# Kernel tuning notes

Hardware: AMD Instinct MI355X
Metric: run time of the kernel (lower is better)

## Reference

```python
import jax, jax.numpy as jnp
import numpy as np

N = 10000
E = 320000

def gcn_layer(x, W, edge_src, edge_dst, edge_weight):
    # support = x @ W ; out = spmm(adj, support) via edge-list scatter-add
    support = x @ W                                  # [N, H]
    msgs = edge_weight[:, None] * support[edge_src]  # [E, H] gather (irregular)
    return jax.ops.segment_sum(msgs, edge_dst, num_segments=N)

def setup_inputs() -> dict:
    key = jax.random.key(0)
    ks = jax.random.split(key, 7)
    F_in, H1, H2 = 3000, 512, 64
    x = jax.random.normal(ks[0], (N, F_in), dtype=jnp.float32)
    edge_src = jax.random.randint(ks[1], (E,), 0, N)
    edge_dst = jax.random.randint(ks[2], (E,), 0, N)
    edge_weight = jax.random.uniform(ks[3], (E,), dtype=jnp.float32)
    W1 = jax.random.normal(ks[4], (F_in, H1), dtype=jnp.float32) * (1.0 / np.sqrt(F_in))
    W2 = jax.random.normal(ks[5], (H1, H2), dtype=jnp.float32) * (1.0 / np.sqrt(H1))
    W3 = jax.random.normal(ks[6], (H1, H2), dtype=jnp.float32) * (1.0 / np.sqrt(H1))
    return {"x": x, "edge_src": edge_src, "edge_dst": edge_dst,
            "edge_weight": edge_weight, "W1": W1, "W2": W2, "W3": W3}

def reference(x, edge_src, edge_dst, edge_weight, W1, W2, W3):
    # Eval mode: dropout is identity, reparameterize returns mu.
    h1 = jax.nn.relu(gcn_layer(x, W1, edge_src, edge_dst, edge_weight))  # [N, H1]
    mu = gcn_layer(h1, W2, edge_src, edge_dst, edge_weight)              # [N, H2]
    logvar = gcn_layer(h1, W3, edge_src, edge_dst, edge_weight)          # [N, H2]
    z = mu
    pred = z @ z.T  # InnerProductDecoder with act = identity -> [N, N]
    return (pred, mu, logvar)
```

## Files before the change

kernel.cpp:

```cpp
#include <hip/hip_runtime.h>
#include <hip/hip_bf16.h>

#define N_NODES 10000
#define N_EDGES 320000
#define F_IN    3000
#define KP      3008
#define H1      512
#define H2      64
#define CAP     128
#define NT      (KP / 32)

typedef float  f32x4  __attribute__((ext_vector_type(4)));
typedef short  bf16x8 __attribute__((ext_vector_type(8)));
typedef unsigned short us8 __attribute__((ext_vector_type(8)));

__device__ __forceinline__ unsigned short f2b(float f) {
    union { float f; unsigned u; } v; v.f = f;
    unsigned r = v.u + 0x7FFF + ((v.u >> 16) & 1);
    return (unsigned short)(r >> 16);
}
__device__ __forceinline__ float b2f(unsigned short b) {
    union { unsigned u; float f; } v; v.u = ((unsigned)b) << 16;
    return v.f;
}

#define GLOAD_LDS16(gptr, lptr)                                                             \
    __builtin_amdgcn_global_load_lds((const __attribute__((address_space(1))) void*)(gptr), \
                                     (__attribute__((address_space(3))) void*)(lptr),       \
                                     16, 0, 0)

#define NB_BUCKET 1250
#define NB_CONVX  14688
#define NB_CONVW  376

__global__ __launch_bounds__(256) void prep(const int* __restrict__ src,
                                            const int* __restrict__ dst,
                                            const float* __restrict__ w,
                                            const float* __restrict__ x,
                                            const float* __restrict__ W1,
                                            int* __restrict__ cnt,
                                            int* __restrict__ bsrc,
                                            float* __restrict__ bw,
                                            unsigned short* __restrict__ xb,
                                            unsigned short* __restrict__ w1t) {
    __shared__ float tr[64][65];
    const int b = blockIdx.x;
    const int t = threadIdx.x;
    if (b < NB_BUCKET) {
        int e = b * 256 + t;
        if (e >= N_EDGES) return;
        int d = dst[e];
        int slot = atomicAdd(&cnt[d], 1);
        if (slot < CAP) {
            bsrc[d * CAP + slot] = src[e];
            bw[d * CAP + slot]   = w[e];
        }
    } else if (b < NB_BUCKET + NB_CONVX) {
        int idx = (b - NB_BUCKET) * 256 + t;
        int r = idx / (KP / 8);
        int g = idx % (KP / 8);
        if (r >= N_NODES) return;
        us8 v;
        if (g * 8 + 8 <= F_IN) {
            float4 a = *(const float4*)&x[(size_t)r * F_IN + g * 8];
            float4 c = *(const float4*)&x[(size_t)r * F_IN + g * 8 + 4];
            v[0] = f2b(a.x); v[1] = f2b(a.y); v[2] = f2b(a.z); v[3] = f2b(a.w);
            v[4] = f2b(c.x); v[5] = f2b(c.y); v[6] = f2b(c.z); v[7] = f2b(c.w);
        } else {
            #pragma unroll
            for (int j = 0; j < 8; ++j) {
                int k = g * 8 + j;
                v[j] = (k < F_IN) ? f2b(x[(size_t)r * F_IN + k]) : (unsigned short)0;
            }
        }
        *(us8*)&xb[(size_t)r * KP + g * 8] = v;
    } else {
        int bb = b - NB_BUCKET - NB_CONVX;
        int kBase = (bb >> 3) * 64;
        int cBase = (bb & 7) * 64;
        int col = cBase + (t & 63);
        #pragma unroll
        for (int i = 0; i < 16; ++i) {
            int row = kBase + i * 4 + (t >> 6);
            float v = (row < F_IN) ? W1[(size_t)row * H1 + col] : 0.f;
            tr[t & 63][i * 4 + (t >> 6)] = v;
        }
        __syncthreads();
        int c = t >> 2, kq = (t & 3) * 16;
        us8 o0, o1;
        #pragma unroll
        for (int j = 0; j < 8; ++j) { o0[j] = f2b(tr[c][kq + j]); o1[j] = f2b(tr[c][kq + 8 + j]); }
        *(us8*)&w1t[(size_t)(cBase + c) * KP + kBase + kq]     = o0;
        *(us8*)&w1t[(size_t)(cBase + c) * KP + kBase + kq + 8] = o1;
    }
}

__global__ __launch_bounds__(256) void gemm1_mfma(const unsigned short* __restrict__ xb,
                                                  const unsigned short* __restrict__ w1t,
                                                  unsigned short* __restrict__ Cb) {
    __shared__ unsigned short As[2][128 * 32];
    __shared__ unsigned short Bs[2][64 * 32];
    const int f  = blockIdx.x;
    const int k8 = f & 7;
    const int j  = f >> 3;
    const int bx = k8 * 10 + (j >> 3);
    const int by = j & 7;
    const int mBase = bx * 128;
    const int nBase = by * 64;

    const int t = threadIdx.x;
    const int wid = t >> 6, lane = t & 63;
    const int wr = (wid >> 1) * 64;
    const int wc = (wid & 1) * 32;
    const int fr = lane & 15;
    const int fk = (lane >> 4) * 8;

    const int arow0 = min(mBase + wid * 16 + (lane >> 2), N_NODES - 1);
    const int arow1 = min(mBase + (wid + 4) * 16 + (lane >> 2), N_NODES - 1);
    const int brow  = nBase + wid * 16 + (lane >> 2);
    const int kq    = (lane & 3) * 8;

    f32x4 acc[4][2] = {};

#define STAGE1(c, k0)                                                          \
    do {                                                                       \
        GLOAD_LDS16(&xb[(size_t)arow0 * KP + (k0) + kq], &As[c][wid * 512]);   \
        GLOAD_LDS16(&xb[(size_t)arow1 * KP + (k0) + kq], &As[c][(wid + 4) * 512]); \
        GLOAD_LDS16(&w1t[(size_t)brow * KP + (k0) + kq], &Bs[c][wid * 512]);   \
    } while (0)

#define COMPUTE1(c)                                                            \
    do {                                                                       \
        bf16x8 af[4], bfv[2];                                                  \
        _Pragma("unroll")                                                      \
        for (int m = 0; m < 4; ++m)                                            \
            af[m] = *(const bf16x8*)&As[c][(wr + m * 16 + fr) * 32 + fk];      \
        _Pragma("unroll")                                                      \
        for (int n = 0; n < 2; ++n)                                            \
            bfv[n] = *(const bf16x8*)&Bs[c][(wc + n * 16 + fr) * 32 + fk];     \
        _Pragma("unroll")                                                      \
        for (int m = 0; m < 4; ++m)                                            \
            _Pragma("unroll")                                                  \
            for (int n = 0; n < 2; ++n)                                        \
                acc[m][n] = __builtin_amdgcn_mfma_f32_16x16x32_bf16(af[m], bfv[n], acc[m][n], 0, 0, 0); \
    } while (0)

    STAGE1(0, 0);
    __syncthreads();
    int cur = 0;
    for (int tt = 0; tt < NT - 1; ++tt) {
        STAGE1(cur ^ 1, (tt + 1) * 32);
        COMPUTE1(cur);
        __syncthreads();
        cur ^= 1;
    }
    COMPUTE1(cur);

#undef STAGE1
#undef COMPUTE1

    #pragma unroll
    for (int m = 0; m < 4; ++m) {
        int rbase = mBase + wr + m * 16 + (lane >> 4) * 4;
        #pragma unroll
        for (int n = 0; n < 2; ++n) {
            int col = nBase + wc + n * 16 + (lane & 15);
            #pragma unroll
            for (int i = 0; i < 4; ++i) {
                int row = rbase + i;
                if (row < N_NODES)
                    Cb[(size_t)row * H1 + col] = f2b(acc[m][n][i]);
            }
        }
    }
}

__global__ __launch_bounds__(256) void gather_h1(const unsigned short* __restrict__ sup,
                                                 const int* __restrict__ cnt,
                                                 const int* __restrict__ bsrc,
                                                 const float* __restrict__ bw,
                                                 float* __restrict__ h1) {
    const int wid  = threadIdx.x >> 6;
    const int lane = threadIdx.x & 63;
    const int n    = blockIdx.x * 4 + wid;
    const int deg  = min(cnt[n], CAP);
    float acc[8] = {};
    for (int e = 0; e < deg; ++e) {
        int   s = bsrc[n * CAP + e];
        float w = bw[n * CAP + e];
        us8 v = *(const us8*)&sup[(size_t)s * H1 + lane * 8];
        #pragma unroll
        for (int j = 0; j < 8; ++j) acc[j] += w * b2f(v[j]);
    }
    float4 o0 = make_float4(fmaxf(acc[0], 0.f), fmaxf(acc[1], 0.f), fmaxf(acc[2], 0.f), fmaxf(acc[3], 0.f));
    float4 o1 = make_float4(fmaxf(acc[4], 0.f), fmaxf(acc[5], 0.f), fmaxf(acc[6], 0.f), fmaxf(acc[7], 0.f));
    *(float4*)&h1[(size_t)n * H1 + lane * 8]     = o0;
    *(float4*)&h1[(size_t)n * H1 + lane * 8 + 4] = o1;
}

__global__ __launch_bounds__(256) void gemm_h1w23(const float* __restrict__ h1,
                                                  const float* __restrict__ W2,
                                                  const float* __restrict__ W3,
                                                  float* __restrict__ sup2) {
    __shared__ float hs[16][H1];
    const int rBase = blockIdx.x * 16;
    const int t = threadIdx.x;
    for (int idx = t * 4; idx < 16 * H1; idx += 256 * 4) {
        int r = idx >> 9;
        int k = idx & 511;
        *(float4*)&hs[r][k] = *(const float4*)&h1[(size_t)(rBase + r) * H1 + k];
    }
    __syncthreads();
    const int col = t & 127;
    const int rg  = (t >> 7) * 8;
    const float* W = (col < 64) ? (W2 + col) : (W3 + (col - 64));
    float acc[8] = {};
    for (int k = 0; k < H1; ++k) {
        float wv = W[k * 64];
        #pragma unroll
        for (int i = 0; i < 8; ++i) acc[i] += wv * hs[rg + i][k];
    }
    #pragma unroll
    for (int i = 0; i < 8; ++i)
        sup2[(size_t)(rBase + rg + i) * 128 + col] = acc[i];
}

__global__ __launch_bounds__(256) void gather_muvar(const float* __restrict__ sup2,
                                                    const int* __restrict__ cnt,
                                                    const int* __restrict__ bsrc,
                                                    const float* __restrict__ bw,
                                                    float* __restrict__ mu,
                                                    float* __restrict__ lv,
                                                    unsigned short* __restrict__ mub) {
    const int n  = blockIdx.x * 8 + (threadIdx.x >> 5);
    const int c4 = (threadIdx.x & 31) * 4;
    const int deg = min(cnt[n], CAP);
    float4 acc = make_float4(0.f, 0.f, 0.f, 0.f);
    for (int e = 0; e < deg; ++e) {
        int   s = bsrc[n * CAP + e];
        float w = bw[n * CAP + e];
        float4 v = *(const float4*)&sup2[(size_t)s * 128 + c4];
        acc.x += w * v.x; acc.y += w * v.y; acc.z += w * v.z; acc.w += w * v.w;
    }
    if (c4 < 64) {
        *(float4*)&mu[(size_t)n * 64 + c4] = acc;
        mub[(size_t)n * 64 + c4 + 0] = f2b(acc.x);
        mub[(size_t)n * 64 + c4 + 1] = f2b(acc.y);
        mub[(size_t)n * 64 + c4 + 2] = f2b(acc.z);
        mub[(size_t)n * 64 + c4 + 3] = f2b(acc.w);
    } else {
        *(float4*)&lv[(size_t)n * 64 + (c4 - 64)] = acc;
    }
}

__global__ __launch_bounds__(256) void pred_mfma(const unsigned short* __restrict__ mub,
                                                 float* __restrict__ pred) {
    __shared__ float st[4][16][68];
    const int t = threadIdx.x, wid = t >> 6, lane = t & 63;
    const int rb = blockIdx.x * 128 + (wid >> 1) * 64;
    const int cb = blockIdx.y * 128 + (wid & 1) * 64;
    const int fr = lane & 15, fk = (lane >> 4) * 8;
    f32x4 acc[4][4] = {};

    #pragma unroll
    for (int ks = 0; ks < 2; ++ks) {
        bf16x8 af[4], bfv[4];
        #pragma unroll
        for (int m = 0; m < 4; ++m) {
            int r = min(rb + m * 16 + fr, N_NODES - 1);
            af[m] = *(const bf16x8*)&mub[(size_t)r * 64 + ks * 32 + fk];
        }
        #pragma unroll
        for (int n = 0; n < 4; ++n) {
            int c = min(cb + n * 16 + fr, N_NODES - 1);
            bfv[n] = *(const bf16x8*)&mub[(size_t)c * 64 + ks * 32 + fk];
        }
        #pragma unroll
        for (int m = 0; m < 4; ++m)
            #pragma unroll
            for (int n = 0; n < 4; ++n)
                acc[m][n] = __builtin_amdgcn_mfma_f32_16x16x32_bf16(af[m], bfv[n], acc[m][n], 0, 0, 0);
    }

    #pragma unroll
    for (int m = 0; m < 4; ++m) {
        #pragma unroll
        for (int n = 0; n < 4; ++n)
            #pragma unroll
            for (int i = 0; i < 4; ++i)
                st[wid][(lane >> 4) * 4 + i][n * 16 + (lane & 15)] = acc[m][n][i];
        int rbase = rb + m * 16;
        #pragma unroll
        for (int it = 0; it < 4; ++it) {
            int row   = it * 4 + (lane >> 4);
            int chunk = lane & 15;
            int grow  = rbase + row;
            int gcol  = cb + chunk * 4;
            if (grow < N_NODES) {
                f32x4 v = *(const f32x4*)&st[wid][row][chunk * 4];
                if (gcol + 3 < N_NODES) {
                    __builtin_nontemporal_store(v, (f32x4*)&pred[(size_t)grow * N_NODES + gcol]);
                } else {
                    #pragma unroll
                    for (int j = 0; j < 4; ++j)
                        if (gcol + j < N_NODES)
                            __builtin_nontemporal_store(v[j], &pred[(size_t)grow * N_NODES + gcol + j]);
                }
            }
        }
    }
}

extern "C" void kernel_launch(void* const* d_in, const int* in_sizes, int n_in,
                              void* d_out, int out_size, void* d_ws, size_t ws_size,
                              hipStream_t stream) {
    const float* x    = (const float*)d_in[0];
    const int*   esrc = (const int*)d_in[1];
    const int*   edst = (const int*)d_in[2];
    const float* ew   = (const float*)d_in[3];
    const float* W1   = (const float*)d_in[4];
    const float* W2   = (const float*)d_in[5];
    const float* W3   = (const float*)d_in[6];

    float* pred = (float*)d_out;
    float* mu   = pred + (size_t)N_NODES * N_NODES;
    float* lv   = mu   + (size_t)N_NODES * H2;

    char* ws = (char*)d_ws;
    unsigned short* sup1b = (unsigned short*)ws; ws += (size_t)N_NODES * H1 * sizeof(short);
    float* h1       = (float*)ws; ws += (size_t)N_NODES * H1 * sizeof(float);
    float* support2 = (float*)ws; ws += (size_t)N_NODES * 2 * H2 * sizeof(float);
    int*   cnt      = (int*)ws;   ws += (size_t)N_NODES * sizeof(int);
    int*   bsrc     = (int*)ws;   ws += (size_t)N_NODES * CAP * sizeof(int);
    float* bw       = (float*)ws; ws += (size_t)N_NODES * CAP * sizeof(float);
    unsigned short* xb  = (unsigned short*)ws; ws += (size_t)N_NODES * KP * sizeof(short);
    unsigned short* w1t = (unsigned short*)ws; ws += (size_t)H1 * KP * sizeof(short);
    unsigned short* mub = (unsigned short*)ws; ws += (size_t)N_NODES * H2 * sizeof(short);

    (void)hipMemsetAsync(cnt, 0, N_NODES * sizeof(int), stream);
    prep<<<NB_BUCKET + NB_CONVX + NB_CONVW, 256, 0, stream>>>(esrc, edst, ew, x, W1,
                                                              cnt, bsrc, bw, xb, w1t);
    gemm1_mfma<<<640, 256, 0, stream>>>(xb, w1t, sup1b);
    gather_h1<<<N_NODES / 4, 256, 0, stream>>>(sup1b, cnt, bsrc, bw, h1);
    gemm_h1w23<<<N_NODES / 16, 256, 0, stream>>>(h1, W2, W3, support2);
    gather_muvar<<<N_NODES / 8, 256, 0, stream>>>(support2, cnt, bsrc, bw, mu, lv, mub);
    pred_mfma<<<dim3((N_NODES + 127) / 128, (N_NODES + 127) / 128), 256, 0, stream>>>(mub, pred);
}
```

Before: 344.5 us.

## Fuse x bf16 conversion into GEMM1 loads and merge gather with W2/W3 GEMM

GEMM1 now reads fp32 x directly, converts it to bf16 in registers and writes it into XOR-swizzled LDS with a K tile of 64. This removes the separate pass that materialised a padded bf16 copy of x. The layer-1 gather is also fused with the h1·[W2|W3] GEMM, so h1 stays in shared memory and never makes a round trip through global memory. In exchange, GEMM1 loads A through registers instead of direct-to-LDS loads, which raises register pressure and may expose more latency on the A operand.

```diff
diff --git a/kernel.cpp b/kernel.cpp
--- a/kernel.cpp
+++ b/kernel.cpp
@@ -8,17 +8,24 @@
 #define H1      512
 #define H2      64
 #define CAP     128
-#define NT      (KP / 32)
+#define BK1     64
+#define NT1     47
 
 typedef float  f32x4  __attribute__((ext_vector_type(4)));
 typedef short  bf16x8 __attribute__((ext_vector_type(8)));
 typedef unsigned short us8 __attribute__((ext_vector_type(8)));
+typedef unsigned int u32x2 __attribute__((ext_vector_type(2)));
 
 __device__ __forceinline__ unsigned short f2b(float f) {
     union { float f; unsigned u; } v; v.f = f;
     unsigned r = v.u + 0x7FFF + ((v.u >> 16) & 1);
     return (unsigned short)(r >> 16);
 }
+__device__ __forceinline__ unsigned short f2b_rne(float f) {
+    union { __hip_bfloat16 h; unsigned short u; } cv;
+    cv.h = __float2bfloat16(f);
+    return cv.u;
+}
 __device__ __forceinline__ float b2f(unsigned short b) {
     union { unsigned u; float f; } v; v.u = ((unsigned)b) << 16;
     return v.f;
@@ -30,18 +37,15 @@
                                      16, 0, 0)
 
 #define NB_BUCKET 1250
-#define NB_CONVX  14688
 #define NB_CONVW  376
 
 __global__ __launch_bounds__(256) void prep(const int* __restrict__ src,
                                             const int* __restrict__ dst,
                                             const float* __restrict__ w,
-                                            const float* __restrict__ x,
                                             const float* __restrict__ W1,
                                             int* __restrict__ cnt,
                                             int* __restrict__ bsrc,
                                             float* __restrict__ bw,
-                                            unsigned short* __restrict__ xb,
                                             unsigned short* __restrict__ w1t) {
     __shared__ float tr[64][65];
     const int b = blockIdx.x;
@@ -55,27 +59,8 @@
             bsrc[d * CAP + slot] = src[e];
             bw[d * CAP + slot]   = w[e];
         }
-    } else if (b < NB_BUCKET + NB_CONVX) {
-        int idx = (b - NB_BUCKET) * 256 + t;
-        int r = idx / (KP / 8);
-        int g = idx % (KP / 8);
-        if (r >= N_NODES) return;
-        us8 v;
-        if (g * 8 + 8 <= F_IN) {
-            float4 a = *(const float4*)&x[(size_t)r * F_IN + g * 8];
-            float4 c = *(const float4*)&x[(size_t)r * F_IN + g * 8 + 4];
-            v[0] = f2b(a.x); v[1] = f2b(a.y); v[2] = f2b(a.z); v[3] = f2b(a.w);
-            v[4] = f2b(c.x); v[5] = f2b(c.y); v[6] = f2b(c.z); v[7] = f2b(c.w);
-        } else {
-            #pragma unroll
-            for (int j = 0; j < 8; ++j) {
-                int k = g * 8 + j;
-                v[j] = (k < F_IN) ? f2b(x[(size_t)r * F_IN + k]) : (unsigned short)0;
-            }
-        }
-        *(us8*)&xb[(size_t)r * KP + g * 8] = v;
     } else {
-        int bb = b - NB_BUCKET - NB_CONVX;
+        int bb = b - NB_BUCKET;
         int kBase = (bb >> 3) * 64;
         int cBase = (bb & 7) * 64;
         int col = cBase + (t & 63);
@@ -95,68 +80,117 @@
     }
 }
 
-__global__ __launch_bounds__(256) void gemm1_mfma(const unsigned short* __restrict__ xb,
+__global__ __launch_bounds__(256) void gemm1_mfma(const float* __restrict__ x,
                                                   const unsigned short* __restrict__ w1t,
                                                   unsigned short* __restrict__ Cb) {
-    __shared__ unsigned short As[2][128 * 32];
-    __shared__ unsigned short Bs[2][64 * 32];
+    __shared__ unsigned short As[2][128 * BK1];
+    __shared__ unsigned short Bs[2][64 * BK1];
     const int f  = blockIdx.x;
     const int k8 = f & 7;
-    const int j  = f >> 3;
-    const int bx = k8 * 10 + (j >> 3);
-    const int by = j & 7;
+    const int jj = f >> 3;
+    const int bx = k8 * 10 + (jj >> 3);
+    const int by = jj & 7;
     const int mBase = bx * 128;
     const int nBase = by * 64;
 
     const int t = threadIdx.x;
     const int wid = t >> 6, lane = t & 63;
-    const int wr = (wid >> 1) * 64;
-    const int wc = (wid & 1) * 32;
-    const int fr = lane & 15;
-    const int fk = (lane >> 4) * 8;
-
-    const int arow0 = min(mBase + wid * 16 + (lane >> 2), N_NODES - 1);
-    const int arow1 = min(mBase + (wid + 4) * 16 + (lane >> 2), N_NODES - 1);
-    const int brow  = nBase + wid * 16 + (lane >> 2);
-    const int kq    = (lane & 3) * 8;
+    const int wr  = (wid >> 1) * 64;
+    const int wc  = (wid & 1) * 32;
+    const int fr  = lane & 15;
+    const int fkb = (lane >> 4) * 16;
+
+    const int l15 = lane & 15;
+    const int arow0 = wid * 32 + (lane >> 4);
+    const int brow_loc = wid * 16 + (lane >> 3);
+    const int bsw      = (((lane & 7) ^ (lane >> 3)) * 16);
 
     f32x4 acc[4][2] = {};
-
-#define STAGE1(c, k0)                                                          \
-    do {                                                                       \
-        GLOAD_LDS16(&xb[(size_t)arow0 * KP + (k0) + kq], &As[c][wid * 512]);   \
-        GLOAD_LDS16(&xb[(size_t)arow1 * KP + (k0) + kq], &As[c][(wid + 4) * 512]); \
-        GLOAD_LDS16(&w1t[(size_t)brow * KP + (k0) + kq], &Bs[c][wid * 512]);   \
+    float4 avf[8];
+
+#define A_LOAD(k0)                                                              \
+    do {                                                                        \
+        const int kk = (k0) + l15 * 4;                                          \
+        const bool ok = kk < F_IN;                                              \
+        _Pragma("unroll")                                                       \
+        for (int it = 0; it < 8; ++it) {                                        \
+            int r = min(mBase + arow0 + it * 4, N_NODES - 1);                   \
+            avf[it] = ok ? *(const float4*)&x[(size_t)r * F_IN + kk]            \
+                         : make_float4(0.f, 0.f, 0.f, 0.f);                     \
+        }                                                                       \
     } while (0)
 
-#define COMPUTE1(c)                                                            \
-    do {                                                                       \
-        bf16x8 af[4], bfv[2];                                                  \
-        _Pragma("unroll")                                                      \
-        for (int m = 0; m < 4; ++m)                                            \
-            af[m] = *(const bf16x8*)&As[c][(wr + m * 16 + fr) * 32 + fk];      \
-        _Pragma("unroll")                                                      \
-        for (int n = 0; n < 2; ++n)                                            \
-            bfv[n] = *(const bf16x8*)&Bs[c][(wc + n * 16 + fr) * 32 + fk];     \
-        _Pragma("unroll")                                                      \
-        for (int m = 0; m < 4; ++m)                                            \
-            _Pragma("unroll")                                                  \
-            for (int n = 0; n < 2; ++n)                                        \
-                acc[m][n] = __builtin_amdgcn_mfma_f32_16x16x32_bf16(af[m], bfv[n], acc[m][n], 0, 0, 0); \
+#define A_WRITE(buf)                                                            \
+    do {                                                                        \
+        _Pragma("unroll")                                                       \
+        for (int it = 0; it < 8; ++it) {                                        \
+            int row = arow0 + it * 4;                                           \
+            unsigned short s0 = f2b_rne(avf[it].x), s1 = f2b_rne(avf[it].y);    \
+            unsigned short s2 = f2b_rne(avf[it].z), s3 = f2b_rne(avf[it].w);    \
+            u32x2 pk; pk[0] = s0 | ((unsigned)s1 << 16);                        \
+            pk[1] = s2 | ((unsigned)s3 << 16);                                  \
+            *(u32x2*)((char*)&As[buf][0] + row * 128 +                          \
+                      ((l15 * 8) ^ ((row & 7) << 4))) = pk;                     \
+        }                                                                       \
     } while (0)
 
-    STAGE1(0, 0);
+#define B_GLOAD(buf, k0)                                                        \
+    do {                                                                        \
+        _Pragma("unroll")                                                       \
+        for (int c = 0; c < 2; ++c) {                                           \
+            const char* gb = (const char*)w1t +                                 \
+                ((size_t)(nBase + brow_loc + c * 8) * KP + (k0)) * 2 + bsw;     \
+            GLOAD_LDS16(gb, (char*)&Bs[buf][0] + wid * 2048 + c * 1024);        \
+        }                                                                       \
+    } while (0)
+
+#define COMPUTE1(buf)                                                           \
+    do {                                                                        \
+        bf16x8 af[4][2], bfv[2][2];                                             \
+        _Pragma("unroll")                                                       \
+        for (int m = 0; m < 4; ++m) {                                           \
+            int row = wr + m * 16 + fr;                                         \
+            _Pragma("unroll")                                                   \
+            for (int ks = 0; ks < 2; ++ks)                                      \
+                af[m][ks] = *(const bf16x8*)((const char*)&As[buf][0] +         \
+                    row * 128 + ((ks * 64 + fkb) ^ ((row & 7) << 4)));          \
+        }                                                                       \
+        _Pragma("unroll")                                                       \
+        for (int n = 0; n < 2; ++n) {                                           \
+            int row = wc + n * 16 + fr;                                         \
+            _Pragma("unroll")                                                   \
+            for (int ks = 0; ks < 2; ++ks)                                      \
+                bfv[n][ks] = *(const bf16x8*)((const char*)&Bs[buf][0] +        \
+                    row * 128 + ((ks * 64 + fkb) ^ ((row & 7) << 4)));          \
+        }                                                                       \
+        _Pragma("unroll")                                                       \
+        for (int ks = 0; ks < 2; ++ks)                                          \
+            _Pragma("unroll")                                                   \
+            for (int m = 0; m < 4; ++m)                                         \
+                _Pragma("unroll")                                               \
+                for (int n = 0; n < 2; ++n)                                     \
+                    acc[m][n] = __builtin_amdgcn_mfma_f32_16x16x32_bf16(        \
+                        af[m][ks], bfv[n][ks], acc[m][n], 0, 0, 0);             \
+    } while (0)
+
+    B_GLOAD(0, 0);
+    A_LOAD(0);
+    A_WRITE(0);
     __syncthreads();
     int cur = 0;
-    for (int tt = 0; tt < NT - 1; ++tt) {
-        STAGE1(cur ^ 1, (tt + 1) * 32);
+    for (int tt = 0; tt < NT1 - 1; ++tt) {
+        B_GLOAD(cur ^ 1, (tt + 1) * BK1);
+        A_LOAD((tt + 1) * BK1);
         COMPUTE1(cur);
+        A_WRITE(cur ^ 1);
         __syncthreads();
         cur ^= 1;
     }
     COMPUTE1(cur);
 
-#undef STAGE1
+#undef A_LOAD
+#undef A_WRITE
+#undef B_GLOAD
 #undef COMPUTE1
 
     #pragma unroll
@@ -175,54 +209,50 @@
     }
 }
 
-__global__ __launch_bounds__(256) void gather_h1(const unsigned short* __restrict__ sup,
-                                                 const int* __restrict__ cnt,
-                                                 const int* __restrict__ bsrc,
-                                                 const float* __restrict__ bw,
-                                                 float* __restrict__ h1) {
-    const int wid  = threadIdx.x >> 6;
-    const int lane = threadIdx.x & 63;
-    const int n    = blockIdx.x * 4 + wid;
-    const int deg  = min(cnt[n], CAP);
-    float acc[8] = {};
-    for (int e = 0; e < deg; ++e) {
-        int   s = bsrc[n * CAP + e];
-        float w = bw[n * CAP + e];
-        us8 v = *(const us8*)&sup[(size_t)s * H1 + lane * 8];
-        #pragma unroll
-        for (int j = 0; j < 8; ++j) acc[j] += w * b2f(v[j]);
-    }
-    float4 o0 = make_float4(fmaxf(acc[0], 0.f), fmaxf(acc[1], 0.f), fmaxf(acc[2], 0.f), fmaxf(acc[3], 0.f));
-    float4 o1 = make_float4(fmaxf(acc[4], 0.f), fmaxf(acc[5], 0.f), fmaxf(acc[6], 0.f), fmaxf(acc[7], 0.f));
-    *(float4*)&h1[(size_t)n * H1 + lane * 8]     = o0;
-    *(float4*)&h1[(size_t)n * H1 + lane * 8 + 4] = o1;
-}
-
-__global__ __launch_bounds__(256) void gemm_h1w23(const float* __restrict__ h1,
-                                                  const float* __restrict__ W2,
-                                                  const float* __restrict__ W3,
-                                                  float* __restrict__ sup2) {
+__global__ __launch_bounds__(512) void gather_gemm23(const unsigned short* __restrict__ sup,
+                                                     const int* __restrict__ cnt,
+                                                     const int* __restrict__ bsrc,
+                                                     const float* __restrict__ bw,
+                                                     const float* __restrict__ W2,
+                                                     const float* __restrict__ W3,
+                                                     float* __restrict__ sup2) {
     __shared__ float hs[16][H1];
+    const int t = threadIdx.x;
+    const int wid = t >> 6, lane = t & 63;
     const int rBase = blockIdx.x * 16;
-    const int t = threadIdx.x;
-    for (int idx = t * 4; idx < 16 * H1; idx += 256 * 4) {
-        int r = idx >> 9;
-        int k = idx & 511;
-        *(float4*)&hs[r][k] = *(const float4*)&h1[(size_t)(rBase + r) * H1 + k];
+
+    #pragma unroll
+    for (int i = 0; i < 2; ++i) {
+        const int local = wid * 2 + i;
+        const int n = rBase + local;
+        const int deg = min(cnt[n], CAP);
+        float acc[8] = {};
+        for (int e = 0; e < deg; ++e) {
+            int   s = bsrc[n * CAP + e];
+            float w = bw[n * CAP + e];
+            us8 v = *(const us8*)&sup[(size_t)s * H1 + lane * 8];
+            #pragma unroll
+            for (int j = 0; j < 8; ++j) acc[j] += w * b2f(v[j]);
+        }
+        *(float4*)&hs[local][lane * 8] =
+            make_float4(fmaxf(acc[0], 0.f), fmaxf(acc[1], 0.f), fmaxf(acc[2], 0.f), fmaxf(acc[3], 0.f));
+        *(float4*)&hs[local][lane * 8 + 4] =
+            make_float4(fmaxf(acc[4], 0.f), fmaxf(acc[5], 0.f), fmaxf(acc[6], 0.f), fmaxf(acc[7], 0.f));
     }
     __syncthreads();
+
     const int col = t & 127;
-    const int rg  = (t >> 7) * 8;
+    const int rg  = (t >> 7) * 4;
     const float* W = (col < 64) ? (W2 + col) : (W3 + (col - 64));
-    float acc[8] = {};
+    float acc2[4] = {};
     for (int k = 0; k < H1; ++k) {
         float wv = W[k * 64];
         #pragma unroll
-        for (int i = 0; i < 8; ++i) acc[i] += wv * hs[rg + i][k];
-    }
-    #pragma unroll
-    for (int i = 0; i < 8; ++i)
-        sup2[(size_t)(rBase + rg + i) * 128 + col] = acc[i];
+        for (int i = 0; i < 4; ++i) acc2[i] += wv * hs[rg + i][k];
+    }
+    #pragma unroll
+    for (int i = 0; i < 4; ++i)
+        sup2[(size_t)(rBase + rg + i) * 128 + col] = acc2[i];
 }
 
 __global__ __launch_bounds__(256) void gather_muvar(const float* __restrict__ sup2,
@@ -328,21 +358,17 @@
 
     char* ws = (char*)d_ws;
     unsigned short* sup1b = (unsigned short*)ws; ws += (size_t)N_NODES * H1 * sizeof(short);
-    float* h1       = (float*)ws; ws += (size_t)N_NODES * H1 * sizeof(float);
     float* support2 = (float*)ws; ws += (size_t)N_NODES * 2 * H2 * sizeof(float);
     int*   cnt      = (int*)ws;   ws += (size_t)N_NODES * sizeof(int);
     int*   bsrc     = (int*)ws;   ws += (size_t)N_NODES * CAP * sizeof(int);
     float* bw       = (float*)ws; ws += (size_t)N_NODES * CAP * sizeof(float);
-    unsigned short* xb  = (unsigned short*)ws; ws += (size_t)N_NODES * KP * sizeof(short);
     unsigned short* w1t = (unsigned short*)ws; ws += (size_t)H1 * KP * sizeof(short);
     unsigned short* mub = (unsigned short*)ws; ws += (size_t)N_NODES * H2 * sizeof(short);
 
     (void)hipMemsetAsync(cnt, 0, N_NODES * sizeof(int), stream);
-    prep<<<NB_BUCKET + NB_CONVX + NB_CONVW, 256, 0, stream>>>(esrc, edst, ew, x, W1,
-                                                              cnt, bsrc, bw, xb, w1t);
-    gemm1_mfma<<<640, 256, 0, stream>>>(xb, w1t, sup1b);
-    gather_h1<<<N_NODES / 4, 256, 0, stream>>>(sup1b, cnt, bsrc, bw, h1);
-    gemm_h1w23<<<N_NODES / 16, 256, 0, stream>>>(h1, W2, W3, support2);
+    prep<<<NB_BUCKET + NB_CONVW, 256, 0, stream>>>(esrc, edst, ew, W1, cnt, bsrc, bw, w1t);
+    gemm1_mfma<<<640, 256, 0, stream>>>(x, w1t, sup1b);
+    gather_gemm23<<<N_NODES / 16, 512, 0, stream>>>(sup1b, cnt, bsrc, bw, W2, W3, support2);
     gather_muvar<<<N_NODES / 8, 256, 0, stream>>>(support2, cnt, bsrc, bw, mu, lv, mub);
     pred_mfma<<<dim3((N_NODES + 127) / 128, (N_NODES + 127) / 128), 256, 0, stream>>>(mub, pred);
 }
```

Result: slower. 389.5 us (+13.1%).

## Fuse layer-1 gather with W2/W3 GEMM and swizzle LDS in gemm1

Applied to the files above, without the earlier changes.

Merges the first-layer edge gather (with ReLU) into the h1×[W2|W3] GEMM kernel. Each 512-thread block gathers 16 node rows straight into shared memory instead of writing and rereading a 20 MB fp32 h1 buffer, which also drops one launch. Separately, gemm1_mfma gets an XOR swizzle on its LDS chunk layout to reduce bank conflicts on fragment reads, plus an occupancy hint of 6 blocks per CU via launch_bounds. The fused kernel has fewer blocks doing more serial gather work per block, which may reduce latency hiding.

```diff
diff --git a/kernel.cpp b/kernel.cpp
--- a/kernel.cpp
+++ b/kernel.cpp
@@ -95,16 +95,16 @@
     }
 }
 
-__global__ __launch_bounds__(256) void gemm1_mfma(const unsigned short* __restrict__ xb,
-                                                  const unsigned short* __restrict__ w1t,
-                                                  unsigned short* __restrict__ Cb) {
+__global__ __launch_bounds__(256, 6) void gemm1_mfma(const unsigned short* __restrict__ xb,
+                                                     const unsigned short* __restrict__ w1t,
+                                                     unsigned short* __restrict__ Cb) {
     __shared__ unsigned short As[2][128 * 32];
     __shared__ unsigned short Bs[2][64 * 32];
     const int f  = blockIdx.x;
     const int k8 = f & 7;
-    const int j  = f >> 3;
-    const int bx = k8 * 10 + (j >> 3);
-    const int by = j & 7;
+    const int jj = f >> 3;
+    const int bx = k8 * 10 + (jj >> 3);
+    const int by = jj & 7;
     const int mBase = bx * 128;
     const int nBase = by * 64;
 
@@ -113,20 +113,21 @@
     const int wr = (wid >> 1) * 64;
     const int wc = (wid & 1) * 32;
     const int fr = lane & 15;
-    const int fk = (lane >> 4) * 8;
-
-    const int arow0 = min(mBase + wid * 16 + (lane >> 2), N_NODES - 1);
-    const int arow1 = min(mBase + (wid + 4) * 16 + (lane >> 2), N_NODES - 1);
-    const int brow  = nBase + wid * 16 + (lane >> 2);
-    const int kq    = (lane & 3) * 8;
+    const int swz = (((lane >> 4) ^ (fr & 3)) << 3);
+
+    const int srow   = lane >> 2;
+    const int schunk = ((lane & 3) ^ (srow & 3)) * 8;
+    const int arow0  = min(mBase + wid * 16 + srow, N_NODES - 1);
+    const int arow1  = min(mBase + (wid + 4) * 16 + srow, N_NODES - 1);
+    const int brow   = nBase + wid * 16 + srow;
 
     f32x4 acc[4][2] = {};
 
-#define STAGE1(c, k0)                                                          \
-    do {                                                                       \
-        GLOAD_LDS16(&xb[(size_t)arow0 * KP + (k0) + kq], &As[c][wid * 512]);   \
-        GLOAD_LDS16(&xb[(size_t)arow1 * KP + (k0) + kq], &As[c][(wid + 4) * 512]); \
-        GLOAD_LDS16(&w1t[(size_t)brow * KP + (k0) + kq], &Bs[c][wid * 512]);   \
+#define STAGE1(c, k0)                                                              \
+    do {                                                                           \
+        GLOAD_LDS16(&xb[(size_t)arow0 * KP + (k0) + schunk], &As[c][wid * 512]);   \
+        GLOAD_LDS16(&xb[(size_t)arow1 * KP + (k0) + schunk], &As[c][(wid + 4) * 512]); \
+        GLOAD_LDS16(&w1t[(size_t)brow * KP + (k0) + schunk], &Bs[c][wid * 512]);   \
     } while (0)
 
 #define COMPUTE1(c)                                                            \
@@ -134,10 +135,10 @@
         bf16x8 af[4], bfv[2];                                                  \
         _Pragma("unroll")                                                      \
         for (int m = 0; m < 4; ++m)                                            \
-            af[m] = *(const bf16x8*)&As[c][(wr + m * 16 + fr) * 32 + fk];      \
+            af[m] = *(const bf16x8*)&As[c][(wr + m * 16 + fr) * 32 + swz];     \
         _Pragma("unroll")                                                      \
         for (int n = 0; n < 2; ++n)                                            \
-            bfv[n] = *(const bf16x8*)&Bs[c][(wc + n * 16 + fr) * 32 + fk];     \
+            bfv[n] = *(const bf16x8*)&Bs[c][(wc + n * 16 + fr) * 32 + swz];    \
         _Pragma("unroll")                                                      \
         for (int m = 0; m < 4; ++m)                                            \
             _Pragma("unroll")                                                  \
@@ -175,54 +176,50 @@
     }
 }
 
-__global__ __launch_bounds__(256) void gather_h1(const unsigned short* __restrict__ sup,
-                                                 const int* __restrict__ cnt,
-                                                 const int* __restrict__ bsrc,
-                                                 const float* __restrict__ bw,
-                                                 float* __restrict__ h1) {
-    const int wid  = threadIdx.x >> 6;
-    const int lane = threadIdx.x & 63;
-    const int n    = blockIdx.x * 4 + wid;
-    const int deg  = min(cnt[n], CAP);
-    float acc[8] = {};
-    for (int e = 0; e < deg; ++e) {
-        int   s = bsrc[n * CAP + e];
-        float w = bw[n * CAP + e];
-        us8 v = *(const us8*)&sup[(size_t)s * H1 + lane * 8];
-        #pragma unroll
-        for (int j = 0; j < 8; ++j) acc[j] += w * b2f(v[j]);
-    }
-    float4 o0 = make_float4(fmaxf(acc[0], 0.f), fmaxf(acc[1], 0.f), fmaxf(acc[2], 0.f), fmaxf(acc[3], 0.f));
-    float4 o1 = make_float4(fmaxf(acc[4], 0.f), fmaxf(acc[5], 0.f), fmaxf(acc[6], 0.f), fmaxf(acc[7], 0.f));
-    *(float4*)&h1[(size_t)n * H1 + lane * 8]     = o0;
-    *(float4*)&h1[(size_t)n * H1 + lane * 8 + 4] = o1;
-}
-
-__global__ __launch_bounds__(256) void gemm_h1w23(const float* __restrict__ h1,
-                                                  const float* __restrict__ W2,
-                                                  const float* __restrict__ W3,
-                                                  float* __restrict__ sup2) {
+__global__ __launch_bounds__(512) void gather_gemm23(const unsigned short* __restrict__ sup,
+                                                     const int* __restrict__ cnt,
+                                                     const int* __restrict__ bsrc,
+                                                     const float* __restrict__ bw,
+                                                     const float* __restrict__ W2,
+                                                     const float* __restrict__ W3,
+                                                     float* __restrict__ sup2) {
     __shared__ float hs[16][H1];
+    const int t = threadIdx.x;
+    const int wid = t >> 6, lane = t & 63;
     const int rBase = blockIdx.x * 16;
-    const int t = threadIdx.x;
-    for (int idx = t * 4; idx < 16 * H1; idx += 256 * 4) {
-        int r = idx >> 9;
-        int k = idx & 511;
-        *(float4*)&hs[r][k] = *(const float4*)&h1[(size_t)(rBase + r) * H1 + k];
+
+    #pragma unroll
+    for (int i = 0; i < 2; ++i) {
+        const int local = wid * 2 + i;
+        const int n = rBase + local;
+        const int deg = min(cnt[n], CAP);
+        float acc[8] = {};
+        for (int e = 0; e < deg; ++e) {
+            int   s = bsrc[n * CAP + e];
+            float w = bw[n * CAP + e];
+            us8 v = *(const us8*)&sup[(size_t)s * H1 + lane * 8];
+            #pragma unroll
+            for (int j = 0; j < 8; ++j) acc[j] += w * b2f(v[j]);
+        }
+        *(float4*)&hs[local][lane * 8] =
+            make_float4(fmaxf(acc[0], 0.f), fmaxf(acc[1], 0.f), fmaxf(acc[2], 0.f), fmaxf(acc[3], 0.f));
+        *(float4*)&hs[local][lane * 8 + 4] =
+            make_float4(fmaxf(acc[4], 0.f), fmaxf(acc[5], 0.f), fmaxf(acc[6], 0.f), fmaxf(acc[7], 0.f));
     }
     __syncthreads();
+
     const int col = t & 127;
-    const int rg  = (t >> 7) * 8;
+    const int rg  = (t >> 7) * 4;
     const float* W = (col < 64) ? (W2 + col) : (W3 + (col - 64));
-    float acc[8] = {};
+    float acc2[4] = {};
     for (int k = 0; k < H1; ++k) {
         float wv = W[k * 64];
         #pragma unroll
-        for (int i = 0; i < 8; ++i) acc[i] += wv * hs[rg + i][k];
-    }
-    #pragma unroll
-    for (int i = 0; i < 8; ++i)
-        sup2[(size_t)(rBase + rg + i) * 128 + col] = acc[i];
+        for (int i = 0; i < 4; ++i) acc2[i] += wv * hs[rg + i][k];
+    }
+    #pragma unroll
+    for (int i = 0; i < 4; ++i)
+        sup2[(size_t)(rBase + rg + i) * 128 + col] = acc2[i];
 }
 
 __global__ __launch_bounds__(256) void gather_muvar(const float* __restrict__ sup2,
@@ -328,7 +325,6 @@
 
     char* ws = (char*)d_ws;
     unsigned short* sup1b = (unsigned short*)ws; ws += (size_t)N_NODES * H1 * sizeof(short);
-    float* h1       = (float*)ws; ws += (size_t)N_NODES * H1 * sizeof(float);
     float* support2 = (float*)ws; ws += (size_t)N_NODES * 2 * H2 * sizeof(float);
     int*   cnt      = (int*)ws;   ws += (size_t)N_NODES * sizeof(int);
     int*   bsrc     = (int*)ws;   ws += (size_t)N_NODES * CAP * sizeof(int);
@@ -341,8 +337,7 @@
     prep<<<NB_BUCKET + NB_CONVX + NB_CONVW, 256, 0, stream>>>(esrc, edst, ew, x, W1,
                                                               cnt, bsrc, bw, xb, w1t);
     gemm1_mfma<<<640, 256, 0, stream>>>(xb, w1t, sup1b);
-    gather_h1<<<N_NODES / 4, 256, 0, stream>>>(sup1b, cnt, bsrc, bw, h1);
-    gemm_h1w23<<<N_NODES / 16, 256, 0, stream>>>(h1, W2, W3, support2);
+    gather_gemm23<<<N_NODES / 16, 512, 0, stream>>>(sup1b, cnt, bsrc, bw, W2, W3, support2);
     gather_muvar<<<N_NODES / 8, 256, 0, stream>>>(support2, cnt, bsrc, bw, mu, lv, mub);
     pred_mfma<<<dim3((N_NODES + 127) / 128, (N_NODES + 127) / 128), 256, 0, stream>>>(mub, pred);
 }
```

Result: no change. 337.8 us (-1.9%).
